# Performance work log

Hardware: AMD Instinct MI355X
Metric: run time of the kernel (lower is better)

Reference implementation:

```python
import jax, jax.numpy as jnp
import numpy as np

N_SRC = 50000
N_DST = 50000
E = 800000
IN_DIM = 128
OUT_DIM = 64
HEADS = 4
NEG_SLOPE = 0.2  # PyG GATConv default negative_slope
EPS = 1e-16      # PyG softmax denominator epsilon


def setup_inputs() -> dict:
    key = jax.random.key(0)
    ks = jax.random.split(key, 8)
    x_src = jax.random.normal(ks[0], (N_SRC, IN_DIM), dtype=jnp.float32)
    x_dst = jax.random.normal(ks[1], (N_DST, IN_DIM), dtype=jnp.float32)
    src = jax.random.randint(ks[2], (E,), 0, N_SRC, dtype=jnp.int32)
    dst = jax.random.randint(ks[3], (E,), 0, N_DST, dtype=jnp.int32)
    edge_index = jnp.stack([src, dst], axis=0)
    W_src = jax.random.normal(ks[4], (IN_DIM, HEADS * OUT_DIM), dtype=jnp.float32) / np.sqrt(IN_DIM)
    W_dst = jax.random.normal(ks[5], (IN_DIM, HEADS * OUT_DIM), dtype=jnp.float32) / np.sqrt(IN_DIM)
    att_src = jax.random.normal(ks[6], (HEADS, OUT_DIM), dtype=jnp.float32) / np.sqrt(OUT_DIM)
    att_dst = jax.random.normal(ks[7], (HEADS, OUT_DIM), dtype=jnp.float32) / np.sqrt(OUT_DIM)
    bias = jnp.zeros((OUT_DIM,), dtype=jnp.float32)
    return {"x_src": x_src, "x_dst": x_dst, "edge_index": edge_index,
            "W_src": W_src, "W_dst": W_dst, "att_src": att_src,
            "att_dst": att_dst, "bias": bias}


def reference(x_src, x_dst, edge_index, W_src, W_dst, att_src, att_dst, bias):
    # Linear projections -> [N, H, C]
    hs = (x_src @ W_src).reshape(N_SRC, HEADS, OUT_DIM)
    hd = (x_dst @ W_dst).reshape(N_DST, HEADS, OUT_DIM)
    # Per-node attention logits -> [N, H]
    a_s = jnp.einsum('nhc,hc->nh', hs, att_src)
    a_d = jnp.einsum('nhc,hc->nh', hd, att_dst)

    src, dst = edge_index[0], edge_index[1]
    # Per-edge logits [E, H]
    alpha = jax.nn.leaky_relu(a_s[src] + a_d[dst], negative_slope=NEG_SLOPE)
    # Segment softmax over edges sharing the same dst node
    amax = jax.ops.segment_max(alpha, dst, num_segments=N_DST)
    alpha = jnp.exp(alpha - amax[dst])
    denom = jax.ops.segment_sum(alpha, dst, num_segments=N_DST)
    alpha = alpha / (denom[dst] + EPS)
    # (dropout=0 / eval mode: no attention dropout)
    # Message + scatter-add aggregation: out[i] = sum_e alpha_e * hs[src_e]
    msg = hs[src] * alpha[:, :, None]                 # [E, H, C]
    out = jax.ops.segment_sum(msg, dst, num_segments=N_DST)  # [N_dst, H, C]
    # concat=False -> mean over heads, then bias
    return out.mean(axis=1) + bias
```

## Files before the change

kernel.cpp:

```cpp
#include <hip/hip_runtime.h>
#include <hip/hip_bf16.h>

#define N_SRC 50000
#define N_DST 50000
#define NEDGE 800000
#define IND   128
#define HEADS 4
#define CDIM  64
#define HC    256
#define MAXDEG 96
#define NB_ALPHA 12500
#define HIST_GPB 256
#define NB_HIST2 2048
#define DPG 6250

typedef _Float16 half8  __attribute__((ext_vector_type(8)));
typedef _Float16 half2t __attribute__((ext_vector_type(2)));
typedef float    f32x4  __attribute__((ext_vector_type(4)));
typedef int      i32x4  __attribute__((ext_vector_type(4)));

static __device__ __forceinline__ unsigned int pack2h(float a, float b) {
    union { half2t h; unsigned int u; } v;
    v.h[0] = (_Float16)a; v.h[1] = (_Float16)b;
    return v.u;
}
static __device__ __forceinline__ half2t bits2h(unsigned int u) {
    union { unsigned int u; half2t h; } v; v.u = u; return v.h;
}

__global__ void prep_kernel(const float* __restrict__ Wdst,
                            const float* __restrict__ att_d,
                            float* __restrict__ WdA,
                            const float* __restrict__ Wsrc,
                            _Float16* __restrict__ WhT, int* __restrict__ deg) {
    int b = blockIdx.x, tid = threadIdx.x;
    if (b < 196) {
        int i = b * 256 + tid;
        if (i < N_DST) deg[i] = 0;
    } else if (b < 198) {
        int id = (b - 196) * 256 + tid;
        int k = id >> 2, h = id & 3;
        float acc = 0.f;
        for (int c = 0; c < CDIM; ++c)
            acc += Wdst[k * HC + h * CDIM + c] * att_d[h * CDIM + c];
        WdA[id] = acc;
    } else {
        int idx = (b - 198) * 256 + tid;
        int n = idx >> 7, k = idx & 127;
        WhT[idx] = (_Float16)Wsrc[k * HC + n];
    }
}

__global__ __launch_bounds__(256) void gemm_mfma_kernel(
        const float* __restrict__ x, const _Float16* __restrict__ WhT,
        const float* __restrict__ att_s,
        unsigned short* __restrict__ hsTh, float* __restrict__ a_s) {
    __shared__ _Float16 sW[256 * 128];
    int tid = threadIdx.x;
    {
        const float4* wsrc = (const float4*)WhT;
        #pragma unroll
        for (int it = 0; it < 16; ++it) {
            int idx = it * 256 + tid;
            int row = idx >> 4, slot = idx & 15;
            float4 v = wsrc[idx];
            int byte_off = row * 256 + ((slot * 16) ^ ((row & 7) << 4));
            *(float4*)((char*)sW + byte_off) = v;
        }
    }

    int w = tid >> 6, lane = tid & 63;
    int ll = lane & 15, q = lane >> 4;
    int rbase = blockIdx.x * 64 + w * 16;

    int arow = rbase + ll;
    if (arow >= N_SRC) arow = N_SRC - 1;
    const float* xr = x + (size_t)arow * IND + q * 8;
    half8 afrag[4];
    #pragma unroll
    for (int kf = 0; kf < 4; ++kf) {
        float4 u0 = *(const float4*)(xr + kf * 32);
        float4 u1 = *(const float4*)(xr + kf * 32 + 4);
        half8 a;
        a[0] = (_Float16)u0.x; a[1] = (_Float16)u0.y;
        a[2] = (_Float16)u0.z; a[3] = (_Float16)u0.w;
        a[4] = (_Float16)u1.x; a[5] = (_Float16)u1.y;
        a[6] = (_Float16)u1.z; a[7] = (_Float16)u1.w;
        afrag[kf] = a;
    }

    f32x4 acc[16];
    #pragma unroll
    for (int t = 0; t < 16; ++t) acc[t] = (f32x4){0.f, 0.f, 0.f, 0.f};

    __syncthreads();
    int sw = (ll & 7) << 4;
    #pragma unroll
    for (int t = 0; t < 16; ++t) {
        const char* rowp = (const char*)sW + (t * 16 + ll) * 256;
        half8 b0 = *(const half8*)(rowp + ((q * 16 +   0) ^ sw));
        half8 b1 = *(const half8*)(rowp + ((q * 16 +  64) ^ sw));
        half8 b2 = *(const half8*)(rowp + ((q * 16 + 128) ^ sw));
        half8 b3 = *(const half8*)(rowp + ((q * 16 + 192) ^ sw));
        f32x4 c = acc[t];
        c = __builtin_amdgcn_mfma_f32_16x16x32_f16(afrag[0], b0, c, 0, 0, 0);
        c = __builtin_amdgcn_mfma_f32_16x16x32_f16(afrag[1], b1, c, 0, 0, 0);
        c = __builtin_amdgcn_mfma_f32_16x16x32_f16(afrag[2], b2, c, 0, 0, 0);
        c = __builtin_amdgcn_mfma_f32_16x16x32_f16(afrag[3], b3, c, 0, 0, 0);
        acc[t] = c;
    }

    #pragma unroll
    for (int tg = 0; tg < 4; ++tg) {
        #pragma unroll
        for (int r = 0; r < 4; ++r) {
            int n = rbase + q * 4 + r;
            if (n < N_SRC) {
                uint2 v;
                v.x = pack2h(acc[tg     ][r], acc[tg + 4 ][r]);
                v.y = pack2h(acc[tg + 8 ][r], acc[tg + 12][r]);
                *(uint2*)(hsTh + (size_t)n * HC + (tg * 16 + ll) * 4) = v;
            }
        }
    }

    float attv[16];
    #pragma unroll
    for (int t = 0; t < 16; ++t) attv[t] = att_s[t * 16 + ll];
    #pragma unroll
    for (int r = 0; r < 4; ++r) {
        float4 p;
        p.x = acc[0][r]*attv[0]  + acc[1][r]*attv[1]  + acc[2][r]*attv[2]  + acc[3][r]*attv[3];
        p.y = acc[4][r]*attv[4]  + acc[5][r]*attv[5]  + acc[6][r]*attv[6]  + acc[7][r]*attv[7];
        p.z = acc[8][r]*attv[8]  + acc[9][r]*attv[9]  + acc[10][r]*attv[10]+ acc[11][r]*attv[11];
        p.w = acc[12][r]*attv[12]+ acc[13][r]*attv[13]+ acc[14][r]*attv[14]+ acc[15][r]*attv[15];
        #pragma unroll
        for (int off = 1; off < 16; off <<= 1) {
            p.x += __shfl_xor(p.x, off, 64);
            p.y += __shfl_xor(p.y, off, 64);
            p.z += __shfl_xor(p.z, off, 64);
            p.w += __shfl_xor(p.w, off, 64);
        }
        int n = rbase + q * 4 + r;
        if (ll == 0 && n < N_SRC) *(float4*)(a_s + (size_t)n * 4) = p;
    }
}

__global__ __launch_bounds__(256) void mid_kernel(
        const float* __restrict__ x_dst, const float* __restrict__ WdA,
        float* __restrict__ a_d,
        const int* __restrict__ src, const int* __restrict__ dst,
        int* __restrict__ deg, int* __restrict__ col2) {
    int b = blockIdx.x, tid = threadIdx.x;
    if (b < NB_HIST2) {
        int g  = b & 7;
        int bg = b >> 3;
        int lo = g * DPG, hi = lo + DPG;
        #pragma unroll 1
        for (int it = 0; it < 4; ++it) {
            int base = ((it * HIST_GPB + bg) << 10) + (tid << 2);
            if (base >= NEDGE) break;
            i32x4 dv = __builtin_nontemporal_load((const i32x4*)(dst + base));
            i32x4 sv = __builtin_nontemporal_load((const i32x4*)(src + base));
            #pragma unroll
            for (int j = 0; j < 4; ++j) {
                int d = dv[j];
                if (d >= lo && d < hi) {
                    int r = atomicAdd(&deg[d], 1);
                    if (r < MAXDEG) col2[d * MAXDEG + r] = sv[j];
                }
            }
        }
    } else {
        int rank = b - NB_HIST2;
        int n    = (rank * 256 + tid) >> 6;
        int lane = tid & 63;
        const float* xp = x_dst + (size_t)n * IND;
        const float4* wa = (const float4*)WdA;
        float x0 = xp[lane], x1 = xp[lane + 64];
        float4 wa0 = wa[lane], wa1 = wa[lane + 64];
        float p0 = x0 * wa0.x + x1 * wa1.x;
        float p1 = x0 * wa0.y + x1 * wa1.y;
        float p2 = x0 * wa0.z + x1 * wa1.z;
        float p3 = x0 * wa0.w + x1 * wa1.w;
        for (int off = 32; off >= 1; off >>= 1) {
            p0 += __shfl_xor(p0, off, 64);
            p1 += __shfl_xor(p1, off, 64);
            p2 += __shfl_xor(p2, off, 64);
            p3 += __shfl_xor(p3, off, 64);
        }
        if (lane == 0) {
            a_d[n * 4 + 0] = p0; a_d[n * 4 + 1] = p1;
            a_d[n * 4 + 2] = p2; a_d[n * 4 + 3] = p3;
        }
    }
}

__global__ __launch_bounds__(256) void aggregate_kernel(
        const int* __restrict__ deg, const int* __restrict__ col2,
        const float4* __restrict__ as4, const float4* __restrict__ ad4,
        const unsigned short* __restrict__ hsTh,
        const float* __restrict__ bias, float* __restrict__ out) {
    __shared__ int   s_off[4][MAXDEG];
    __shared__ uint4 s_pk[4][MAXDEG];
    int tid = threadIdx.x;
    int wv = tid >> 6, lane = tid & 63;
    int i = (blockIdx.x * 256 + tid) >> 6;
    if (i >= N_DST) return;
    int dg = deg[i]; if (dg > MAXDEG) dg = MAXDEG;
    float bv = bias[lane];
    if (dg == 0) { out[i * CDIM + lane] = bv; return; }
    float4 ad = ad4[i];
    const int* crow = col2 + i * MAXDEG;

    float s0 = 0.f, s1 = 0.f, s2 = 0.f, s3 = 0.f;
    for (int e = lane; e < dg; e += 64) {
        int sn = crow[e];
        float4 av = as4[sn];
        float lx = av.x + ad.x; lx = lx > 0.f ? lx : 0.2f * lx;
        float ly = av.y + ad.y; ly = ly > 0.f ? ly : 0.2f * ly;
        float lz = av.z + ad.z; lz = lz > 0.f ? lz : 0.2f * lz;
        float lw = av.w + ad.w; lw = lw > 0.f ? lw : 0.2f * lw;
        float w0 = __expf(lx), w1 = __expf(ly), w2 = __expf(lz), w3 = __expf(lw);
        s0 += w0; s1 += w1; s2 += w2; s3 += w3;
        s_off[wv][e] = sn * HC;
        float4 wf = {w0, w1, w2, w3};
        *(float4*)&s_pk[wv][e] = wf;
    }
    for (int off = 32; off >= 1; off >>= 1) {
        s0 += __shfl_xor(s0, off, 64);
        s1 += __shfl_xor(s1, off, 64);
        s2 += __shfl_xor(s2, off, 64);
        s3 += __shfl_xor(s3, off, 64);
    }
    float i0 = 0.25f / (s0 + 1e-16f);
    float i1 = 0.25f / (s1 + 1e-16f);
    float i2 = 0.25f / (s2 + 1e-16f);
    float i3 = 0.25f / (s3 + 1e-16f);

    for (int e = lane; e < dg; e += 64) {
        float4 wf = *(float4*)&s_pk[wv][e];
        uint4 pk;
        pk.x = (unsigned int)s_off[wv][e];
        pk.y = pack2h(wf.x * i0, wf.y * i1);
        pk.z = pack2h(wf.z * i2, wf.w * i3);
        pk.w = 0;
        s_pk[wv][e] = pk;
    }
    __asm__ volatile("s_waitcnt lgkmcnt(0)" ::: "memory");

    const unsigned short* hb = hsTh + (lane << 2);
    float acc = 0.f;
    int j = 0;
    for (; j + 4 <= dg; j += 4) {
        uint4 p0 = s_pk[wv][j];
        uint4 p1 = s_pk[wv][j + 1];
        uint4 p2 = s_pk[wv][j + 2];
        uint4 p3 = s_pk[wv][j + 3];
        uint2 h0 = *(const uint2*)(hb + p0.x);
        uint2 h1 = *(const uint2*)(hb + p1.x);
        uint2 h2 = *(const uint2*)(hb + p2.x);
        uint2 h3 = *(const uint2*)(hb + p3.x);
        acc = __builtin_amdgcn_fdot2(bits2h(h0.x), bits2h(p0.y), acc, false);
        acc = __builtin_amdgcn_fdot2(bits2h(h0.y), bits2h(p0.z), acc, false);
        acc = __builtin_amdgcn_fdot2(bits2h(h1.x), bits2h(p1.y), acc, false);
        acc = __builtin_amdgcn_fdot2(bits2h(h1.y), bits2h(p1.z), acc, false);
        acc = __builtin_amdgcn_fdot2(bits2h(h2.x), bits2h(p2.y), acc, false);
        acc = __builtin_amdgcn_fdot2(bits2h(h2.y), bits2h(p2.z), acc, false);
        acc = __builtin_amdgcn_fdot2(bits2h(h3.x), bits2h(p3.y), acc, false);
        acc = __builtin_amdgcn_fdot2(bits2h(h3.y), bits2h(p3.z), acc, false);
    }
    for (; j < dg; ++j) {
        uint4 p0 = s_pk[wv][j];
        uint2 h0 = *(const uint2*)(hb + p0.x);
        acc = __builtin_amdgcn_fdot2(bits2h(h0.x), bits2h(p0.y), acc, false);
        acc = __builtin_amdgcn_fdot2(bits2h(h0.y), bits2h(p0.z), acc, false);
    }
    out[i * CDIM + lane] = acc + bv;
}

extern "C" void kernel_launch(void* const* d_in, const int* in_sizes, int n_in,
                              void* d_out, int out_size, void* d_ws, size_t ws_size,
                              hipStream_t stream) {
    const float* x_src   = (const float*)d_in[0];
    const float* x_dst   = (const float*)d_in[1];
    const int*   ei      = (const int*)d_in[2];
    const float* W_src   = (const float*)d_in[3];
    const float* W_dst   = (const float*)d_in[4];
    const float* att_src = (const float*)d_in[5];
    const float* att_dst = (const float*)d_in[6];
    const float* bias    = (const float*)d_in[7];
    float* out = (float*)d_out;

    char* ws = (char*)d_ws;
    unsigned short* hsTh = (unsigned short*)ws; ws += (size_t)N_SRC * HC * 2;
    int*    col2    = (int*)ws;    ws += (size_t)N_DST * MAXDEG * 4;
    float*  a_s     = (float*)ws;  ws += (size_t)N_SRC * 4 * 4;
    float*  a_d     = (float*)ws;  ws += (size_t)N_DST * 4 * 4;
    float*  WdA     = (float*)ws;  ws += 2048;
    _Float16* WhT   = (_Float16*)ws; ws += IND * HC * 2;
    int*    deg     = (int*)ws;    ws += N_DST * 4;

    prep_kernel<<<326, 256, 0, stream>>>(W_dst, att_dst, WdA, W_src, WhT, deg);
    gemm_mfma_kernel<<<(N_SRC + 63) / 64, 256, 0, stream>>>(x_src, WhT, att_src, hsTh, a_s);
    mid_kernel<<<NB_HIST2 + NB_ALPHA, 256, 0, stream>>>(x_dst, WdA, a_d, ei, ei + NEDGE, deg, col2);
    aggregate_kernel<<<(N_DST + 3) / 4, 256, 0, stream>>>(deg, col2,
                                                          (const float4*)a_s, (const float4*)a_d,
                                                          hsTh, bias, out);
}
```

Measured before the change: 220.5 us.

## Aggregate raw fp16 source features then apply projection GEMM per destination

Reorders the computation so each destination first aggregates attention-weighted fp16 input features (128-dim, per head) into a 512-wide z vector. A final MFMA GEMM against a rearranged W_src with head-mean folded in then produces the output. Source attention logits are now computed from x_src with W_src·att_s folded into a vector, which removes the full hs projection GEMM. The aim is to shrink the per-edge gather from 256 fp16 projected values to 128 fp16 raw features and to drop the separate source GEMM. In exchange it adds a z intermediate of 50k×512 fp16, an extra GEMM kernel, and more FMAs per edge in aggregation.

```diff
diff --git a/kernel.cpp b/kernel.cpp
--- a/kernel.cpp
+++ b/kernel.cpp
@@ -8,11 +8,13 @@
 #define HEADS 4
 #define CDIM  64
 #define HC    256
+#define KTOT  512
 #define MAXDEG 96
 #define NB_ALPHA 12500
 #define HIST_GPB 256
 #define NB_HIST2 2048
 #define DPG 6250
+#define NB_CAST 3125
 
 typedef _Float16 half8  __attribute__((ext_vector_type(8)));
 typedef _Float16 half2t __attribute__((ext_vector_type(2)));
@@ -32,7 +34,12 @@
                             const float* __restrict__ att_d,
                             float* __restrict__ WdA,
                             const float* __restrict__ Wsrc,
-                            _Float16* __restrict__ WhT, int* __restrict__ deg) {
+                            const float* __restrict__ att_s,
+                            float* __restrict__ WsA,
+                            _Float16* __restrict__ WfT,
+                            const float* __restrict__ x_src,
+                            _Float16* __restrict__ xh,
+                            int* __restrict__ deg) {
     int b = blockIdx.x, tid = threadIdx.x;
     if (b < 196) {
         int i = b * 256 + tid;
@@ -44,111 +51,37 @@
         for (int c = 0; c < CDIM; ++c)
             acc += Wdst[k * HC + h * CDIM + c] * att_d[h * CDIM + c];
         WdA[id] = acc;
+    } else if (b < 200) {
+        int id = (b - 198) * 256 + tid;
+        int k = id >> 2, h = id & 3;
+        float acc = 0.f;
+        for (int c = 0; c < CDIM; ++c)
+            acc += Wsrc[k * HC + h * CDIM + c] * att_s[h * CDIM + c];
+        WsA[id] = acc;
+    } else if (b < 328) {
+        int idx = (b - 200) * 256 + tid;
+        int c = idx >> 9, hk = idx & 511;
+        int h = hk >> 7, k = hk & 127;
+        WfT[idx] = (_Float16)Wsrc[k * HC + h * CDIM + c];
     } else {
-        int idx = (b - 198) * 256 + tid;
-        int n = idx >> 7, k = idx & 127;
-        WhT[idx] = (_Float16)Wsrc[k * HC + n];
-    }
-}
-
-__global__ __launch_bounds__(256) void gemm_mfma_kernel(
-        const float* __restrict__ x, const _Float16* __restrict__ WhT,
-        const float* __restrict__ att_s,
-        unsigned short* __restrict__ hsTh, float* __restrict__ a_s) {
-    __shared__ _Float16 sW[256 * 128];
-    int tid = threadIdx.x;
-    {
-        const float4* wsrc = (const float4*)WhT;
-        #pragma unroll
-        for (int it = 0; it < 16; ++it) {
-            int idx = it * 256 + tid;
-            int row = idx >> 4, slot = idx & 15;
-            float4 v = wsrc[idx];
-            int byte_off = row * 256 + ((slot * 16) ^ ((row & 7) << 4));
-            *(float4*)((char*)sW + byte_off) = v;
-        }
-    }
-
-    int w = tid >> 6, lane = tid & 63;
-    int ll = lane & 15, q = lane >> 4;
-    int rbase = blockIdx.x * 64 + w * 16;
-
-    int arow = rbase + ll;
-    if (arow >= N_SRC) arow = N_SRC - 1;
-    const float* xr = x + (size_t)arow * IND + q * 8;
-    half8 afrag[4];
-    #pragma unroll
-    for (int kf = 0; kf < 4; ++kf) {
-        float4 u0 = *(const float4*)(xr + kf * 32);
-        float4 u1 = *(const float4*)(xr + kf * 32 + 4);
-        half8 a;
-        a[0] = (_Float16)u0.x; a[1] = (_Float16)u0.y;
-        a[2] = (_Float16)u0.z; a[3] = (_Float16)u0.w;
-        a[4] = (_Float16)u1.x; a[5] = (_Float16)u1.y;
-        a[6] = (_Float16)u1.z; a[7] = (_Float16)u1.w;
-        afrag[kf] = a;
-    }
-
-    f32x4 acc[16];
-    #pragma unroll
-    for (int t = 0; t < 16; ++t) acc[t] = (f32x4){0.f, 0.f, 0.f, 0.f};
-
-    __syncthreads();
-    int sw = (ll & 7) << 4;
-    #pragma unroll
-    for (int t = 0; t < 16; ++t) {
-        const char* rowp = (const char*)sW + (t * 16 + ll) * 256;
-        half8 b0 = *(const half8*)(rowp + ((q * 16 +   0) ^ sw));
-        half8 b1 = *(const half8*)(rowp + ((q * 16 +  64) ^ sw));
-        half8 b2 = *(const half8*)(rowp + ((q * 16 + 128) ^ sw));
-        half8 b3 = *(const half8*)(rowp + ((q * 16 + 192) ^ sw));
-        f32x4 c = acc[t];
-        c = __builtin_amdgcn_mfma_f32_16x16x32_f16(afrag[0], b0, c, 0, 0, 0);
-        c = __builtin_amdgcn_mfma_f32_16x16x32_f16(afrag[1], b1, c, 0, 0, 0);
-        c = __builtin_amdgcn_mfma_f32_16x16x32_f16(afrag[2], b2, c, 0, 0, 0);
-        c = __builtin_amdgcn_mfma_f32_16x16x32_f16(afrag[3], b3, c, 0, 0, 0);
-        acc[t] = c;
-    }
-
-    #pragma unroll
-    for (int tg = 0; tg < 4; ++tg) {
-        #pragma unroll
-        for (int r = 0; r < 4; ++r) {
-            int n = rbase + q * 4 + r;
-            if (n < N_SRC) {
-                uint2 v;
-                v.x = pack2h(acc[tg     ][r], acc[tg + 4 ][r]);
-                v.y = pack2h(acc[tg + 8 ][r], acc[tg + 12][r]);
-                *(uint2*)(hsTh + (size_t)n * HC + (tg * 16 + ll) * 4) = v;
-            }
-        }
-    }
-
-    float attv[16];
-    #pragma unroll
-    for (int t = 0; t < 16; ++t) attv[t] = att_s[t * 16 + ll];
-    #pragma unroll
-    for (int r = 0; r < 4; ++r) {
-        float4 p;
-        p.x = acc[0][r]*attv[0]  + acc[1][r]*attv[1]  + acc[2][r]*attv[2]  + acc[3][r]*attv[3];
-        p.y = acc[4][r]*attv[4]  + acc[5][r]*attv[5]  + acc[6][r]*attv[6]  + acc[7][r]*attv[7];
-        p.z = acc[8][r]*attv[8]  + acc[9][r]*attv[9]  + acc[10][r]*attv[10]+ acc[11][r]*attv[11];
-        p.w = acc[12][r]*attv[12]+ acc[13][r]*attv[13]+ acc[14][r]*attv[14]+ acc[15][r]*attv[15];
-        #pragma unroll
-        for (int off = 1; off < 16; off <<= 1) {
-            p.x += __shfl_xor(p.x, off, 64);
-            p.y += __shfl_xor(p.y, off, 64);
-            p.z += __shfl_xor(p.z, off, 64);
-            p.w += __shfl_xor(p.w, off, 64);
-        }
-        int n = rbase + q * 4 + r;
-        if (ll == 0 && n < N_SRC) *(float4*)(a_s + (size_t)n * 4) = p;
+        int e = (b - 328) * 256 + tid;
+        const float* xp = x_src + (size_t)e * 8;
+        float4 u0 = *(const float4*)(xp);
+        float4 u1 = *(const float4*)(xp + 4);
+        half8 v;
+        v[0] = (_Float16)u0.x; v[1] = (_Float16)u0.y;
+        v[2] = (_Float16)u0.z; v[3] = (_Float16)u0.w;
+        v[4] = (_Float16)u1.x; v[5] = (_Float16)u1.y;
+        v[6] = (_Float16)u1.z; v[7] = (_Float16)u1.w;
+        *(half8*)(xh + (size_t)e * 8) = v;
     }
 }
 
 __global__ __launch_bounds__(256) void mid_kernel(
         const float* __restrict__ x_dst, const float* __restrict__ WdA,
         float* __restrict__ a_d,
+        const float* __restrict__ x_src, const float* __restrict__ WsA,
+        float* __restrict__ a_s,
         const int* __restrict__ src, const int* __restrict__ dst,
         int* __restrict__ deg, int* __restrict__ col2) {
     int b = blockIdx.x, tid = threadIdx.x;
@@ -173,10 +106,16 @@
         }
     } else {
         int rank = b - NB_HIST2;
+        const float* xbase; const float4* wa; float* outp;
+        if (rank < NB_ALPHA) {
+            xbase = x_dst; wa = (const float4*)WdA; outp = a_d;
+        } else {
+            rank -= NB_ALPHA;
+            xbase = x_src; wa = (const float4*)WsA; outp = a_s;
+        }
         int n    = (rank * 256 + tid) >> 6;
         int lane = tid & 63;
-        const float* xp = x_dst + (size_t)n * IND;
-        const float4* wa = (const float4*)WdA;
+        const float* xp = xbase + (size_t)n * IND;
         float x0 = xp[lane], x1 = xp[lane + 64];
         float4 wa0 = wa[lane], wa1 = wa[lane + 64];
         float p0 = x0 * wa0.x + x1 * wa1.x;
@@ -190,8 +129,8 @@
             p3 += __shfl_xor(p3, off, 64);
         }
         if (lane == 0) {
-            a_d[n * 4 + 0] = p0; a_d[n * 4 + 1] = p1;
-            a_d[n * 4 + 2] = p2; a_d[n * 4 + 3] = p3;
+            outp[n * 4 + 0] = p0; outp[n * 4 + 1] = p1;
+            outp[n * 4 + 2] = p2; outp[n * 4 + 3] = p3;
         }
     }
 }
@@ -199,17 +138,20 @@
 __global__ __launch_bounds__(256) void aggregate_kernel(
         const int* __restrict__ deg, const int* __restrict__ col2,
         const float4* __restrict__ as4, const float4* __restrict__ ad4,
-        const unsigned short* __restrict__ hsTh,
-        const float* __restrict__ bias, float* __restrict__ out) {
-    __shared__ int   s_off[4][MAXDEG];
-    __shared__ uint4 s_pk[4][MAXDEG];
+        const unsigned int* __restrict__ xh32,
+        unsigned int* __restrict__ z32) {
+    __shared__ int    s_off[4][MAXDEG];
+    __shared__ float4 s_w[4][MAXDEG];
     int tid = threadIdx.x;
     int wv = tid >> 6, lane = tid & 63;
     int i = (blockIdx.x * 256 + tid) >> 6;
     if (i >= N_DST) return;
     int dg = deg[i]; if (dg > MAXDEG) dg = MAXDEG;
-    float bv = bias[lane];
-    if (dg == 0) { out[i * CDIM + lane] = bv; return; }
+    unsigned int* zo = z32 + (size_t)i * 256 + lane;
+    if (dg == 0) {
+        zo[0] = 0u; zo[64] = 0u; zo[128] = 0u; zo[192] = 0u;
+        return;
+    }
     float4 ad = ad4[i];
     const int* crow = col2 + i * MAXDEG;
 
@@ -223,9 +165,8 @@
         float lw = av.w + ad.w; lw = lw > 0.f ? lw : 0.2f * lw;
         float w0 = __expf(lx), w1 = __expf(ly), w2 = __expf(lz), w3 = __expf(lw);
         s0 += w0; s1 += w1; s2 += w2; s3 += w3;
-        s_off[wv][e] = sn * HC;
-        float4 wf = {w0, w1, w2, w3};
-        *(float4*)&s_pk[wv][e] = wf;
+        s_off[wv][e] = sn;
+        s_w[wv][e] = (float4){w0, w1, w2, w3};
     }
     for (int off = 32; off >= 1; off >>= 1) {
         s0 += __shfl_xor(s0, off, 64);
@@ -239,44 +180,114 @@
     float i3 = 0.25f / (s3 + 1e-16f);
 
     for (int e = lane; e < dg; e += 64) {
-        float4 wf = *(float4*)&s_pk[wv][e];
-        uint4 pk;
-        pk.x = (unsigned int)s_off[wv][e];
-        pk.y = pack2h(wf.x * i0, wf.y * i1);
-        pk.z = pack2h(wf.z * i2, wf.w * i3);
-        pk.w = 0;
-        s_pk[wv][e] = pk;
+        float4 wf = s_w[wv][e];
+        wf.x *= i0; wf.y *= i1; wf.z *= i2; wf.w *= i3;
+        s_w[wv][e] = wf;
     }
     __asm__ volatile("s_waitcnt lgkmcnt(0)" ::: "memory");
 
-    const unsigned short* hb = hsTh + (lane << 2);
-    float acc = 0.f;
+    const unsigned int* xb = xh32 + lane;
+    float z00 = 0.f, z01 = 0.f, z10 = 0.f, z11 = 0.f;
+    float z20 = 0.f, z21 = 0.f, z30 = 0.f, z31 = 0.f;
     int j = 0;
     for (; j + 4 <= dg; j += 4) {
-        uint4 p0 = s_pk[wv][j];
-        uint4 p1 = s_pk[wv][j + 1];
-        uint4 p2 = s_pk[wv][j + 2];
-        uint4 p3 = s_pk[wv][j + 3];
-        uint2 h0 = *(const uint2*)(hb + p0.x);
-        uint2 h1 = *(const uint2*)(hb + p1.x);
-        uint2 h2 = *(const uint2*)(hb + p2.x);
-        uint2 h3 = *(const uint2*)(hb + p3.x);
-        acc = __builtin_amdgcn_fdot2(bits2h(h0.x), bits2h(p0.y), acc, false);
-        acc = __builtin_amdgcn_fdot2(bits2h(h0.y), bits2h(p0.z), acc, false);
-        acc = __builtin_amdgcn_fdot2(bits2h(h1.x), bits2h(p1.y), acc, false);
-        acc = __builtin_amdgcn_fdot2(bits2h(h1.y), bits2h(p1.z), acc, false);
-        acc = __builtin_amdgcn_fdot2(bits2h(h2.x), bits2h(p2.y), acc, false);
-        acc = __builtin_amdgcn_fdot2(bits2h(h2.y), bits2h(p2.z), acc, false);
-        acc = __builtin_amdgcn_fdot2(bits2h(h3.x), bits2h(p3.y), acc, false);
-        acc = __builtin_amdgcn_fdot2(bits2h(h3.y), bits2h(p3.z), acc, false);
+        int sn0 = s_off[wv][j],     sn1 = s_off[wv][j + 1];
+        int sn2 = s_off[wv][j + 2], sn3 = s_off[wv][j + 3];
+        float4 w0 = s_w[wv][j],     w1 = s_w[wv][j + 1];
+        float4 w2 = s_w[wv][j + 2], w3 = s_w[wv][j + 3];
+        unsigned int g0 = xb[sn0 << 6];
+        unsigned int g1 = xb[sn1 << 6];
+        unsigned int g2 = xb[sn2 << 6];
+        unsigned int g3 = xb[sn3 << 6];
+        half2t hx;
+        hx = bits2h(g0);
+        { float xa = (float)hx[0], xb2 = (float)hx[1];
+          z00 += w0.x * xa; z01 += w0.x * xb2; z10 += w0.y * xa; z11 += w0.y * xb2;
+          z20 += w0.z * xa; z21 += w0.z * xb2; z30 += w0.w * xa; z31 += w0.w * xb2; }
+        hx = bits2h(g1);
+        { float xa = (float)hx[0], xb2 = (float)hx[1];
+          z00 += w1.x * xa; z01 += w1.x * xb2; z10 += w1.y * xa; z11 += w1.y * xb2;
+          z20 += w1.z * xa; z21 += w1.z * xb2; z30 += w1.w * xa; z31 += w1.w * xb2; }
+        hx = bits2h(g2);
+        { float xa = (float)hx[0], xb2 = (float)hx[1];
+          z00 += w2.x * xa; z01 += w2.x * xb2; z10 += w2.y * xa; z11 += w2.y * xb2;
+          z20 += w2.z * xa; z21 += w2.z * xb2; z30 += w2.w * xa; z31 += w2.w * xb2; }
+        hx = bits2h(g3);
+        { float xa = (float)hx[0], xb2 = (float)hx[1];
+          z00 += w3.x * xa; z01 += w3.x * xb2; z10 += w3.y * xa; z11 += w3.y * xb2;
+          z20 += w3.z * xa; z21 += w3.z * xb2; z30 += w3.w * xa; z31 += w3.w * xb2; }
     }
     for (; j < dg; ++j) {
-        uint4 p0 = s_pk[wv][j];
-        uint2 h0 = *(const uint2*)(hb + p0.x);
-        acc = __builtin_amdgcn_fdot2(bits2h(h0.x), bits2h(p0.y), acc, false);
-        acc = __builtin_amdgcn_fdot2(bits2h(h0.y), bits2h(p0.z), acc, false);
-    }
-    out[i * CDIM + lane] = acc + bv;
+        int sn0 = s_off[wv][j];
+        float4 w0 = s_w[wv][j];
+        unsigned int g0 = xb[sn0 << 6];
+        half2t hx = bits2h(g0);
+        float xa = (float)hx[0], xb2 = (float)hx[1];
+        z00 += w0.x * xa; z01 += w0.x * xb2; z10 += w0.y * xa; z11 += w0.y * xb2;
+        z20 += w0.z * xa; z21 += w0.z * xb2; z30 += w0.w * xa; z31 += w0.w * xb2;
+    }
+    zo[0]   = pack2h(z00, z01);
+    zo[64]  = pack2h(z10, z11);
+    zo[128] = pack2h(z20, z21);
+    zo[192] = pack2h(z30, z31);
+}
+
+__global__ __launch_bounds__(256) void fgemm_kernel(
+        const _Float16* __restrict__ z, const _Float16* __restrict__ WfT,
+        const float* __restrict__ bias, float* __restrict__ out) {
+    __shared__ _Float16 sW[64 * KTOT];
+    int tid = threadIdx.x;
+    {
+        const float4* wsrc = (const float4*)WfT;
+        #pragma unroll
+        for (int it = 0; it < 16; ++it) {
+            int idx = it * 256 + tid;
+            int row = idx >> 6, slot = idx & 63;
+            float4 v = wsrc[idx];
+            int byte_off = row * 1024 + ((slot * 16) ^ ((row & 7) << 4));
+            *(float4*)((char*)sW + byte_off) = v;
+        }
+    }
+
+    int w = tid >> 6, lane = tid & 63;
+    int ll = lane & 15, q = lane >> 4;
+    int rbase = blockIdx.x * 64 + w * 16;
+
+    int arow = rbase + ll;
+    if (arow >= N_DST) arow = N_DST - 1;
+    const _Float16* zr = z + (size_t)arow * KTOT + q * 8;
+    half8 afrag[16];
+    #pragma unroll
+    for (int s = 0; s < 16; ++s)
+        afrag[s] = *(const half8*)(zr + s * 32);
+
+    f32x4 acc[4];
+    #pragma unroll
+    for (int t = 0; t < 4; ++t) acc[t] = (f32x4){0.f, 0.f, 0.f, 0.f};
+
+    __syncthreads();
+    int sw = (ll & 7) << 4;
+    #pragma unroll
+    for (int t = 0; t < 4; ++t) {
+        const char* rowp = (const char*)sW + (t * 16 + ll) * 1024;
+        f32x4 c = acc[t];
+        #pragma unroll
+        for (int s = 0; s < 16; ++s) {
+            half8 bb = *(const half8*)(rowp + ((s * 64 + q * 16) ^ sw));
+            c = __builtin_amdgcn_mfma_f32_16x16x32_f16(afrag[s], bb, c, 0, 0, 0);
+        }
+        acc[t] = c;
+    }
+
+    #pragma unroll
+    for (int t = 0; t < 4; ++t) {
+        float bv = bias[t * 16 + ll];
+        #pragma unroll
+        for (int r = 0; r < 4; ++r) {
+            int n = rbase + q * 4 + r;
+            if (n < N_DST) out[(size_t)n * CDIM + t * 16 + ll] = acc[t][r] + bv;
+        }
+    }
 }
 
 extern "C" void kernel_launch(void* const* d_in, const int* in_sizes, int n_in,
@@ -293,18 +304,23 @@
     float* out = (float*)d_out;
 
     char* ws = (char*)d_ws;
-    unsigned short* hsTh = (unsigned short*)ws; ws += (size_t)N_SRC * HC * 2;
-    int*    col2    = (int*)ws;    ws += (size_t)N_DST * MAXDEG * 4;
-    float*  a_s     = (float*)ws;  ws += (size_t)N_SRC * 4 * 4;
-    float*  a_d     = (float*)ws;  ws += (size_t)N_DST * 4 * 4;
-    float*  WdA     = (float*)ws;  ws += 2048;
-    _Float16* WhT   = (_Float16*)ws; ws += IND * HC * 2;
-    int*    deg     = (int*)ws;    ws += N_DST * 4;
-
-    prep_kernel<<<326, 256, 0, stream>>>(W_dst, att_dst, WdA, W_src, WhT, deg);
-    gemm_mfma_kernel<<<(N_SRC + 63) / 64, 256, 0, stream>>>(x_src, WhT, att_src, hsTh, a_s);
-    mid_kernel<<<NB_HIST2 + NB_ALPHA, 256, 0, stream>>>(x_dst, WdA, a_d, ei, ei + NEDGE, deg, col2);
-    aggregate_kernel<<<(N_DST + 3) / 4, 256, 0, stream>>>(deg, col2,
-                                                          (const float4*)a_s, (const float4*)a_d,
-                                                          hsTh, bias, out);
-}
+    _Float16* xh   = (_Float16*)ws; ws += (size_t)N_SRC * IND * 2;
+    _Float16* z    = (_Float16*)ws; ws += (size_t)N_DST * KTOT * 2;
+    int*    col2   = (int*)ws;    ws += (size_t)N_DST * MAXDEG * 4;
+    float*  a_s    = (float*)ws;  ws += (size_t)N_SRC * 4 * 4;
+    float*  a_d    = (float*)ws;  ws += (size_t)N_DST * 4 * 4;
+    float*  WdA    = (float*)ws;  ws += 2048;
+    float*  WsA    = (float*)ws;  ws += 2048;
+    _Float16* WfT  = (_Float16*)ws; ws += (size_t)CDIM * KTOT * 2;
+    int*    deg    = (int*)ws;    ws += N_DST * 4;
+
+    prep_kernel<<<328 + NB_CAST, 256, 0, stream>>>(W_dst, att_dst, WdA,
+                                                   W_src, att_src, WsA, WfT,
+                                                   x_src, xh, deg);
+    mid_kernel<<<NB_HIST2 + 2 * NB_ALPHA, 256, 0, stream>>>(
+            x_dst, WdA, a_d, x_src, WsA, a_s, ei, ei + NEDGE, deg, col2);
+    aggregate_kernel<<<(N_DST + 3) / 4, 256, 0, stream>>>(
+            deg, col2, (const float4*)a_s, (const float4*)a_d,
+            (const unsigned int*)xh, (unsigned int*)z);
+    fgemm_kernel<<<(N_DST + 63) / 64, 256, 0, stream>>>(z, WfT, bias, out);
+}
```

Result: no change. 220.5 us (-0.0%).
